# Optimization experiments

Hardware: AMD Instinct MI355X
Metric: run time of the kernel (lower is better)

Reference implementation:

```python
import jax, jax.numpy as jnp
import numpy as np

EMBED_DIM = 2048
NUM_HEADS = 16
B, L = 1, 4096


def setup_inputs() -> dict:
    key = jax.random.key(0)
    ks = jax.random.split(key, 6)
    s = 1.0 / np.sqrt(EMBED_DIM)
    return {
        "hidden_states": jax.random.normal(ks[0], (B, L, EMBED_DIM), jnp.float32),
        "Wq": jax.random.normal(ks[1], (EMBED_DIM, EMBED_DIM), jnp.float32) * s,
        "bq": jnp.zeros((EMBED_DIM,), jnp.float32),
        "Wk": jax.random.normal(ks[2], (EMBED_DIM, EMBED_DIM), jnp.float32) * s,
        "bk": jnp.zeros((EMBED_DIM,), jnp.float32),
        "Wv": jax.random.normal(ks[3], (EMBED_DIM, EMBED_DIM), jnp.float32) * s,
        "bv": jnp.zeros((EMBED_DIM,), jnp.float32),
        "Wo": jax.random.normal(ks[4], (EMBED_DIM, EMBED_DIM), jnp.float32) * s,
        "bo": jnp.zeros((EMBED_DIM,), jnp.float32),
        "is_causal": 1,
    }


def reference(hidden_states, Wq, bq, Wk, bk, Wv, bv, Wo, bo, is_causal):
    Bc, Lc, D = hidden_states.shape
    H = NUM_HEADS
    Dh = D // H
    scale = Dh ** (-0.5)

    def proj(W, b):
        # torch Linear: x @ W.T + b; reshape to [B, H, L, Dh]
        y = jnp.einsum('bld,ed->ble', hidden_states, W) + b
        return y.reshape(Bc, Lc, H, Dh).transpose(0, 2, 1, 3)

    q = proj(Wq, bq)
    k = proj(Wk, bk)
    v = proj(Wv, bv)

    scores = jnp.einsum('bhqd,bhkd->bhqk', q, k) * scale  # [B,H,L,L]
    if is_causal:
        causal = jnp.triu(jnp.ones((Lc, Lc), dtype=bool), k=1)
        scores = jnp.where(causal, -jnp.inf, scores)
    w = jax.nn.softmax(scores, axis=-1)
    attn = jnp.einsum('bhqk,bhkd->bhqd', w, v)
    attn = attn.transpose(0, 2, 1, 3).reshape(Bc, Lc, D)
    return jnp.einsum('bld,ed->ble', attn, Wo) + bo
```

## Files before the change

### kernel.cpp

```cpp
#include <hip/hip_runtime.h>
#include <hip/hip_bf16.h>

typedef unsigned short u16;
typedef __attribute__((ext_vector_type(8))) short short8;
typedef __attribute__((ext_vector_type(4))) float f32x4;

#define L 4096
#define DMODEL 2048
#define NHEADS 16
#define DHEAD 128
#define QSCALE (0.08838834764831845f * 1.44269504088896340f)

__device__ __forceinline__ u16 f2bf(float f){
  union { float f; unsigned int i; } v; v.f = f;
  unsigned int u = v.i;
  u += 0x7fffu + ((u >> 16) & 1u);
  return (u16)(u >> 16);
}

__device__ __forceinline__ unsigned int cvtpk(float lo, float hi){
  unsigned int d;
  asm("v_cvt_pk_bf16_f32 %0, %1, %2" : "=v"(d) : "v"(lo), "v"(hi));
  return d;
}

__global__ void cast_kernel(const float* __restrict__ in, u16* __restrict__ out, int n){
  int stride = gridDim.x * blockDim.x * 4;
  for (int j = (blockIdx.x * blockDim.x + threadIdx.x) * 4; j < n; j += stride){
    float4 f = *reinterpret_cast<const float4*>(in + j);
    ushort4 o;
    o.x = f2bf(f.x); o.y = f2bf(f.y); o.z = f2bf(f.z); o.w = f2bf(f.w);
    *reinterpret_cast<ushort4*>(out + j) = o;
  }
}

__global__ void cast_w4_kernel(const float* __restrict__ w0, const float* __restrict__ w1,
                               const float* __restrict__ w2, const float* __restrict__ w3,
                               u16* __restrict__ o0, u16* __restrict__ o1,
                               u16* __restrict__ o2, u16* __restrict__ o3){
  const float* in = (blockIdx.y == 0) ? w0 : (blockIdx.y == 1) ? w1 : (blockIdx.y == 2) ? w2 : w3;
  u16* out = (blockIdx.y == 0) ? o0 : (blockIdx.y == 1) ? o1 : (blockIdx.y == 2) ? o2 : o3;
  const int n = DMODEL * DMODEL;
  int stride = gridDim.x * blockDim.x * 4;
  for (int j = (blockIdx.x * blockDim.x + threadIdx.x) * 4; j < n; j += stride){
    float4 f = *reinterpret_cast<const float4*>(in + j);
    ushort4 o;
    o.x = f2bf(f.x); o.y = f2bf(f.y); o.z = f2bf(f.z); o.w = f2bf(f.w);
    *reinterpret_cast<ushort4*>(out + j) = o;
  }
}

__device__ __forceinline__ void gl_lds16(void* lds, const void* g){
  __builtin_amdgcn_global_load_lds(
      (const __attribute__((address_space(1))) unsigned int*)g,
      (__attribute__((address_space(3))) unsigned int*)lds, 16, 0, 0);
}

#define GBUF (24576)

__global__ __launch_bounds__(512, 2) void gemm_qkv(const u16* __restrict__ A,
    const u16* __restrict__ Wq, const u16* __restrict__ Wk, const u16* __restrict__ Wv,
    const float* __restrict__ bq, const float* __restrict__ bk, const float* __restrict__ bv,
    u16* __restrict__ Qb, u16* __restrict__ Kb, u16* __restrict__ Vtb){
  extern __shared__ u16 gsm[];
  const int tid = threadIdx.x;
  const int wid = tid >> 6, lane = tid & 63;
  const int wm = wid >> 2, wn = wid & 3;
  const int g = lane >> 4, r = lane & 15;
  const int bx = blockIdx.x;
  const int sel = blockIdx.y >> 4;
  const int byl = blockIdx.y & 15;

  const u16* W      = (sel == 0) ? Wq : (sel == 1) ? Wk : Wv;
  const float* bias = (sel == 0) ? bq : (sel == 1) ? bk : bv;
  const float cscale = (sel == 0) ? QSCALE : 1.0f;

  const int srow = tid >> 3;
  const int sc = ((tid & 7) * 16) ^ ((srow & 7) << 4);
  const u16* Ag = A + ((size_t)(bx * 256) + srow) * DMODEL + (sc >> 1);
  const u16* Bg = W + ((size_t)(byl * 128) + srow) * DMODEL + (sc >> 1);
  const int ldsw = wid * 1024;

  f32x4 acc[8][2];
  #pragma unroll
  for (int m = 0; m < 8; ++m){ acc[m][0] = (f32x4){0,0,0,0}; acc[m][1] = (f32x4){0,0,0,0}; }

  const int NK = DMODEL / 64;

  auto STAGE = [&](int b, int tk){
    char* ab = (char*)(gsm + b * GBUF);
    char* bb = (char*)(gsm + b * GBUF + 16384);
    const int ke = tk * 64;
    #pragma unroll
    for (int i = 0; i < 4; ++i)
      gl_lds16(ab + i * 8192 + ldsw, (const char*)(Ag + (size_t)i * 64 * DMODEL + ke));
    #pragma unroll
    for (int i = 0; i < 2; ++i)
      gl_lds16(bb + i * 8192 + ldsw, (const char*)(Bg + (size_t)i * 64 * DMODEL + ke));
  };

  STAGE(0, 0); STAGE(1, 1);

  for (int t = 0; t < NK; ++t){
    if (t < NK - 1) asm volatile("s_waitcnt vmcnt(6)" ::: "memory");
    else            asm volatile("s_waitcnt vmcnt(0)" ::: "memory");
    __builtin_amdgcn_sched_barrier(0);
    __builtin_amdgcn_s_barrier();
    __builtin_amdgcn_sched_barrier(0);

    if (t + 2 < NK) STAGE((t + 2) % 3, t + 2);

    const char* ab = (const char*)(gsm + (t % 3) * GBUF);
    const char* bb = (const char*)(gsm + (t % 3) * GBUF + 16384);

    short8 af[8][2], bf[2][2];
    #pragma unroll
    for (int mt = 0; mt < 8; ++mt){
      const int ar = wm * 128 + mt * 16 + r;
      #pragma unroll
      for (int ks = 0; ks < 2; ++ks)
        af[mt][ks] = *reinterpret_cast<const short8*>(
            ab + ar * 128 + ((ks * 64 + g * 16) ^ ((ar & 7) << 4)));
    }
    #pragma unroll
    for (int nt = 0; nt < 2; ++nt){
      const int br = wn * 32 + nt * 16 + r;
      #pragma unroll
      for (int ks = 0; ks < 2; ++ks)
        bf[nt][ks] = *reinterpret_cast<const short8*>(
            bb + br * 128 + ((ks * 64 + g * 16) ^ ((br & 7) << 4)));
    }

    __builtin_amdgcn_s_setprio(1);
    #pragma unroll
    for (int mt = 0; mt < 8; ++mt)
      #pragma unroll
      for (int nt = 0; nt < 2; ++nt)
        #pragma unroll
        for (int ks = 0; ks < 2; ++ks)
          acc[mt][nt] = __builtin_amdgcn_mfma_f32_16x16x32_bf16(af[mt][ks], bf[nt][ks], acc[mt][nt], 0, 0, 0);
    __builtin_amdgcn_s_setprio(0);
  }

  #pragma unroll
  for (int nt = 0; nt < 2; ++nt){
    const int col = byl * 128 + wn * 32 + nt * 16 + r;
    const float bv = bias[col];
    #pragma unroll
    for (int mt = 0; mt < 8; ++mt){
      #pragma unroll
      for (int qi = 0; qi < 4; ++qi){
        const int row = bx * 256 + wm * 128 + mt * 16 + g * 4 + qi;
        const u16 hb = f2bf((acc[mt][nt][qi] + bv) * cscale);
        if (sel < 2){
          u16* outp = (sel == 0) ? Qb : Kb;
          outp[(size_t)(col >> 7) * (L * DHEAD) + (size_t)row * DHEAD + (col & 127)] = hb;
        } else {
          Vtb[(size_t)(col >> 7) * (DHEAD * L) + (size_t)(col & 127) * L + row] = hb;
        }
      }
    }
  }
}

__global__ __launch_bounds__(512, 2) void gemm_o(const u16* __restrict__ A, const u16* __restrict__ W,
                                                 const float* __restrict__ bias, float* __restrict__ outp){
  extern __shared__ u16 gsm[];
  const int tid = threadIdx.x;
  const int wid = tid >> 6, lane = tid & 63;
  const int wm = wid >> 2, wn = wid & 3;
  const int g = lane >> 4, r = lane & 15;
  const int bx = blockIdx.x, by = blockIdx.y;

  const int srow = tid >> 3;
  const int sc = ((tid & 7) * 16) ^ ((srow & 7) << 4);
  const u16* Ag = A + ((size_t)(bx * 256) + srow) * DMODEL + (sc >> 1);
  const u16* Bg = W + ((size_t)(by * 128) + srow) * DMODEL + (sc >> 1);
  const int ldsw = wid * 1024;

  f32x4 acc[8][2];
  #pragma unroll
  for (int m = 0; m < 8; ++m){ acc[m][0] = (f32x4){0,0,0,0}; acc[m][1] = (f32x4){0,0,0,0}; }

  const int NK = DMODEL / 64;

  auto STAGE = [&](int b, int tk){
    char* ab = (char*)(gsm + b * GBUF);
    char* bb = (char*)(gsm + b * GBUF + 16384);
    const int ke = tk * 64;
    #pragma unroll
    for (int i = 0; i < 4; ++i)
      gl_lds16(ab + i * 8192 + ldsw, (const char*)(Ag + (size_t)i * 64 * DMODEL + ke));
    #pragma unroll
    for (int i = 0; i < 2; ++i)
      gl_lds16(bb + i * 8192 + ldsw, (const char*)(Bg + (size_t)i * 64 * DMODEL + ke));
  };

  STAGE(0, 0); STAGE(1, 1);

  for (int t = 0; t < NK; ++t){
    if (t < NK - 1) asm volatile("s_waitcnt vmcnt(6)" ::: "memory");
    else            asm volatile("s_waitcnt vmcnt(0)" ::: "memory");
    __builtin_amdgcn_sched_barrier(0);
    __builtin_amdgcn_s_barrier();
    __builtin_amdgcn_sched_barrier(0);

    if (t + 2 < NK) STAGE((t + 2) % 3, t + 2);

    const char* ab = (const char*)(gsm + (t % 3) * GBUF);
    const char* bb = (const char*)(gsm + (t % 3) * GBUF + 16384);

    short8 af[8][2], bf[2][2];
    #pragma unroll
    for (int mt = 0; mt < 8; ++mt){
      const int ar = wm * 128 + mt * 16 + r;
      #pragma unroll
      for (int ks = 0; ks < 2; ++ks)
        af[mt][ks] = *reinterpret_cast<const short8*>(
            ab + ar * 128 + ((ks * 64 + g * 16) ^ ((ar & 7) << 4)));
    }
    #pragma unroll
    for (int nt = 0; nt < 2; ++nt){
      const int br = wn * 32 + nt * 16 + r;
      #pragma unroll
      for (int ks = 0; ks < 2; ++ks)
        bf[nt][ks] = *reinterpret_cast<const short8*>(
            bb + br * 128 + ((ks * 64 + g * 16) ^ ((br & 7) << 4)));
    }

    __builtin_amdgcn_s_setprio(1);
    #pragma unroll
    for (int mt = 0; mt < 8; ++mt)
      #pragma unroll
      for (int nt = 0; nt < 2; ++nt)
        #pragma unroll
        for (int ks = 0; ks < 2; ++ks)
          acc[mt][nt] = __builtin_amdgcn_mfma_f32_16x16x32_bf16(af[mt][ks], bf[nt][ks], acc[mt][nt], 0, 0, 0);
    __builtin_amdgcn_s_setprio(0);
  }

  #pragma unroll
  for (int nt = 0; nt < 2; ++nt){
    const int col = by * 128 + wn * 32 + nt * 16 + r;
    const float bv = bias[col];
    #pragma unroll
    for (int mt = 0; mt < 8; ++mt){
      #pragma unroll
      for (int qi = 0; qi < 4; ++qi){
        const int row = bx * 256 + wm * 128 + mt * 16 + g * 4 + qi;
        outp[(size_t)row * DMODEL + col] = acc[mt][nt][qi] + bv;
      }
    }
  }
}


__device__ __forceinline__ void stage_K64(u16* buf, const u16* Kh, int kv0, int wid, int lane){
  #pragma unroll
  for (int i = 0; i < 4; ++i){
    int ib = (wid * 4 + i) * 1024;
    int off = ib + lane * 16;
    int row = off >> 8;
    int c = off & 255;
    int sc = c ^ ((row & 7) << 4);
    gl_lds16((char*)buf + ib, (const char*)(Kh + (size_t)(kv0 + row) * DHEAD) + sc);
  }
}

__device__ __forceinline__ void stage_V64(u16* buf, const u16* Vh, int kv0, int wid, int lane){
  #pragma unroll
  for (int i = 0; i < 4; ++i){
    int ib = (wid * 4 + i) * 1024;
    int off = ib + lane * 16;
    int row = off >> 7;
    int c = off & 127;
    int sc = c ^ ((row & 7) << 4);
    gl_lds16((char*)buf + ib, (const char*)(Vh + (size_t)row * L + kv0) + sc);
  }
}

__device__ __forceinline__ void sm_F(f32x4 (&s)[4], float &l, bool dg, int qrow,
                                     int kv0, int g, int r, char* Pw, int prow0){
  if (dg){
    #pragma unroll
    for (int cb = 0; cb < 4; ++cb){
      int kvb = kv0 + cb * 16 + g * 4;
      #pragma unroll
      for (int e = 0; e < 4; ++e)
        if (kvb + e > qrow) s[cb][e] = -1e30f;
    }
  }
  float rs = 0.f;
  uint2 pkv[4];
  #pragma unroll
  for (int cb = 0; cb < 4; ++cb){
    float p0 = __builtin_amdgcn_exp2f(s[cb][0]);
    float p1 = __builtin_amdgcn_exp2f(s[cb][1]);
    float p2 = __builtin_amdgcn_exp2f(s[cb][2]);
    float p3 = __builtin_amdgcn_exp2f(s[cb][3]);
    rs += (p0 + p1) + (p2 + p3);
    pkv[cb].x = cvtpk(p0, p1);
    pkv[cb].y = cvtpk(p2, p3);
  }
  rs += __shfl_xor(rs, 16);
  rs += __shfl_xor(rs, 32);
  l += rs;
  const int row = prow0 + r;
  char* base = Pw + row * 128;
  #pragma unroll
  for (int cb = 0; cb < 4; ++cb)
    *reinterpret_cast<uint2*>(base + ((cb * 32 + g * 8) ^ ((row & 7) << 4))) = pkv[cb];
}

__global__ __launch_bounds__(256, 2) void attn_kernel(const u16* __restrict__ Q, const u16* __restrict__ Km,
                                                      const u16* __restrict__ Vt, u16* __restrict__ Ob,
                                                      const int* __restrict__ is_causal_p){
  extern __shared__ u16 smem[];
  u16* Ks  = smem;
  u16* Vsm = smem + 16384;
  u16* Ps  = smem + 32768;

  const int lane = threadIdx.x & 63, wid = threadIdx.x >> 6;
  const int g = lane >> 4, r = lane & 15;

  int lg = (blockIdx.x & 7) * 64 + (blockIdx.x >> 3);
  int head = lg >> 5;
  int raw = lg & 31;
  int j = (head & 1) ? (31 - raw) : raw;
  const int jA = j, jB = 63 - j;
  const int causal = *is_causal_p;
  const int nt = causal ? (jB + 1) : 64;

  const u16* Qh = Q  + (size_t)head * L * DHEAD;
  const u16* Kh = Km + (size_t)head * L * DHEAD;
  const u16* Vh = Vt + (size_t)head * DHEAD * L;
  char* Pw = (char*)(Ps + wid * 2048);

  const int rowA = 64 * jA + wid * 16;
  const int rowB = 64 * jB + wid * 16;

  short8 qf[2][4];
  #pragma unroll
  for (int kb = 0; kb < 4; ++kb){
    qf[0][kb] = *reinterpret_cast<const short8*>(&Qh[(size_t)(rowA + r) * DHEAD + kb * 32 + g * 8]);
    qf[1][kb] = *reinterpret_cast<const short8*>(&Qh[(size_t)(rowB + r) * DHEAD + kb * 32 + g * 8]);
  }

  f32x4 o[2][8];
  #pragma unroll
  for (int m = 0; m < 2; ++m)
    #pragma unroll
    for (int db = 0; db < 8; ++db) o[m][db] = (f32x4){0.f, 0.f, 0.f, 0.f};
  float lA = 0.f, lB = 0.f;

  stage_K64(Ks,  Kh, 0, wid, lane);
  stage_V64(Vsm, Vh, 0, wid, lane);

  for (int t = 0; t < nt; ++t){
    const int kv0 = t * 64;
    const bool actA = (!causal) || (t <= jA);
    const bool dgA = causal && (t == jA);
    const bool dgB = causal && (t == jB);

    asm volatile("s_waitcnt vmcnt(0)" ::: "memory");
    __builtin_amdgcn_sched_barrier(0);
    __builtin_amdgcn_s_barrier();
    __builtin_amdgcn_sched_barrier(0);

    if (t + 1 < nt){
      stage_K64(Ks  + ((t + 1) & 1) * 8192, Kh, kv0 + 64, wid, lane);
      stage_V64(Vsm + ((t + 1) & 1) * 8192, Vh, kv0 + 64, wid, lane);
    }

    const char* Kb = (const char*)(Ks  + (t & 1) * 8192);
    const char* Vb = (const char*)(Vsm + (t & 1) * 8192);

    f32x4 s[2][4];
    #pragma unroll
    for (int m = 0; m < 2; ++m)
      #pragma unroll
      for (int cb = 0; cb < 4; ++cb) s[m][cb] = (f32x4){-16.f, -16.f, -16.f, -16.f};
    __builtin_amdgcn_s_setprio(1);
    #pragma unroll
    for (int cb = 0; cb < 4; ++cb){
      const int rr = cb * 16 + r;
      short8 kf[4];
      #pragma unroll
      for (int kb = 0; kb < 4; ++kb)
        kf[kb] = *reinterpret_cast<const short8*>(
            Kb + rr * 256 + ((kb * 64 + g * 16) ^ ((rr & 7) << 4)));
      if (actA){
        #pragma unroll
        for (int kb = 0; kb < 4; ++kb)
          s[0][cb] = __builtin_amdgcn_mfma_f32_16x16x32_bf16(kf[kb], qf[0][kb], s[0][cb], 0, 0, 0);
      }
      #pragma unroll
      for (int kb = 0; kb < 4; ++kb)
        s[1][cb] = __builtin_amdgcn_mfma_f32_16x16x32_bf16(kf[kb], qf[1][kb], s[1][cb], 0, 0, 0);
    }
    __builtin_amdgcn_s_setprio(0);

    if (actA) sm_F(s[0], lA, dgA, rowA + r, kv0, g, r, Pw, 0);
    sm_F(s[1], lB, dgB, rowB + r, kv0, g, r, Pw, 16);

    __builtin_amdgcn_s_setprio(1);
    #pragma unroll
    for (int st = 0; st < 2; ++st){
      short8 vf[8];
      #pragma unroll
      for (int db = 0; db < 8; ++db){
        const int rv = db * 16 + r;
        vf[db] = *reinterpret_cast<const short8*>(
            Vb + rv * 128 + (((st * 32 + g * 8) * 2) ^ ((rv & 7) << 4)));
      }
      if (st == 0){
        asm volatile("s_waitcnt lgkmcnt(0)" ::: "memory");
        __builtin_amdgcn_sched_barrier(0);
      }
      short8 pa0, pa1;
      if (actA)
        pa0 = *reinterpret_cast<const short8*>(
            Pw + r * 128 + ((st * 64 + g * 16) ^ ((r & 7) << 4)));
      pa1 = *reinterpret_cast<const short8*>(
          Pw + (16 + r) * 128 + ((st * 64 + g * 16) ^ ((r & 7) << 4)));
      #pragma unroll
      for (int db = 0; db < 8; ++db){
        if (actA)
          o[0][db] = __builtin_amdgcn_mfma_f32_16x16x32_bf16(pa0, vf[db], o[0][db], 0, 0, 0);
        o[1][db] = __builtin_amdgcn_mfma_f32_16x16x32_bf16(pa1, vf[db], o[1][db], 0, 0, 0);
      }
    }
    __builtin_amdgcn_s_setprio(0);
  }

  #pragma unroll
  for (int m = 0; m < 2; ++m){
    const int rbase = m ? rowB : rowA;
    const float lv = m ? lB : lA;
    float lb[4];
    #pragma unroll
    for (int qi = 0; qi < 4; ++qi) lb[qi] = __shfl(lv, g * 4 + qi);
    #pragma unroll
    for (int db = 0; db < 8; ++db)
      #pragma unroll
      for (int qi = 0; qi < 4; ++qi){
        float val = o[m][db][qi] / lb[qi];
        int qrow = rbase + g * 4 + qi;
        Ob[(size_t)qrow * DMODEL + head * DHEAD + db * 16 + r] = f2bf(val);
      }
  }
}

extern "C" void kernel_launch(void* const* d_in, const int* in_sizes, int n_in,
                              void* d_out, int out_size, void* d_ws, size_t ws_size,
                              hipStream_t stream){
  const float* X  = (const float*)d_in[0];
  const float* Wq = (const float*)d_in[1];
  const float* bq = (const float*)d_in[2];
  const float* Wk = (const float*)d_in[3];
  const float* bk = (const float*)d_in[4];
  const float* Wv = (const float*)d_in[5];
  const float* bv = (const float*)d_in[6];
  const float* Wo = (const float*)d_in[7];
  const float* bo = (const float*)d_in[8];
  const int*   isc = (const int*)d_in[9];

  char* ws = (char*)d_ws;
  u16* Xb  = (u16*)(ws);
  u16* Qb  = (u16*)(ws + 16777216);
  u16* Kb  = (u16*)(ws + 33554432);
  u16* Vtb = (u16*)(ws + 50331648);
  u16* Wqb = (u16*)(ws + 67108864);
  u16* Wkb = (u16*)(ws + 75497472);
  u16* Wvb = (u16*)(ws + 83886080);
  u16* Wob = (u16*)(ws + 92274688);
  u16* Ob  = Xb;

  (void)hipFuncSetAttribute(reinterpret_cast<const void*>(attn_kernel),
                            hipFuncAttributeMaxDynamicSharedMemorySize, 81920);
  (void)hipFuncSetAttribute(reinterpret_cast<const void*>(gemm_qkv),
                            hipFuncAttributeMaxDynamicSharedMemorySize, 147456);
  (void)hipFuncSetAttribute(reinterpret_cast<const void*>(gemm_o),
                            hipFuncAttributeMaxDynamicSharedMemorySize, 147456);

  cast_kernel<<<2048, 256, 0, stream>>>(X, Xb, L * DMODEL);
  cast_w4_kernel<<<dim3(1024, 4), 256, 0, stream>>>(Wq, Wk, Wv, Wo, Wqb, Wkb, Wvb, Wob);

  gemm_qkv<<<dim3(16, 48), 512, 147456, stream>>>(Xb, Wqb, Wkb, Wvb, bq, bk, bv, Qb, Kb, Vtb);

  attn_kernel<<<512, 256, 81920, stream>>>(Qb, Kb, Vtb, Ob, isc);

  gemm_o<<<dim3(16, 16), 512, 147456, stream>>>(Ob, Wob, bo, (float*)d_out);
}
```

Before: 299.7 us.

## Shrink attention KV tiles to 32 and split paired query blocks across waves

The attention kernel now uses 32-row KV tiles and 32-row query blocks. Instead of each wave handling both query blocks of a causal-balanced pair, two waves take the low block and two take the high block, each holding one Q fragment and one accumulator set. Shared memory drops to 36 KB, the grid doubles to 1024 blocks and launch bounds allow 4 blocks per CU, aiming for higher occupancy and lower register pressure. The cost is twice as many barrier iterations per unit of work, less K/V reuse per LDS load, and idle waves in the low-block half during steps past its causal limit.

```diff
diff --git a/kernel.cpp b/kernel.cpp
--- a/kernel.cpp
+++ b/kernel.cpp
@@ -255,10 +255,10 @@
 }
 
 
-__device__ __forceinline__ void stage_K64(u16* buf, const u16* Kh, int kv0, int wid, int lane){
-  #pragma unroll
-  for (int i = 0; i < 4; ++i){
-    int ib = (wid * 4 + i) * 1024;
+__device__ __forceinline__ void stage_K32(u16* buf, const u16* Kh, int kv0, int wid, int lane){
+  #pragma unroll
+  for (int i = 0; i < 2; ++i){
+    int ib = (wid * 2 + i) * 1024;
     int off = ib + lane * 16;
     int row = off >> 8;
     int c = off & 255;
@@ -267,23 +267,23 @@
   }
 }
 
-__device__ __forceinline__ void stage_V64(u16* buf, const u16* Vh, int kv0, int wid, int lane){
-  #pragma unroll
-  for (int i = 0; i < 4; ++i){
-    int ib = (wid * 4 + i) * 1024;
+__device__ __forceinline__ void stage_V32(u16* buf, const u16* Vh, int kv0, int wid, int lane){
+  #pragma unroll
+  for (int i = 0; i < 2; ++i){
+    int ib = (wid * 2 + i) * 1024;
     int off = ib + lane * 16;
-    int row = off >> 7;
-    int c = off & 127;
-    int sc = c ^ ((row & 7) << 4);
+    int row = off >> 6;
+    int c = off & 63;
+    int sc = c ^ ((row & 3) << 4);
     gl_lds16((char*)buf + ib, (const char*)(Vh + (size_t)row * L + kv0) + sc);
   }
 }
 
-__device__ __forceinline__ void sm_F(f32x4 (&s)[4], float &l, bool dg, int qrow,
-                                     int kv0, int g, int r, char* Pw, int prow0){
+__device__ __forceinline__ void sm_F(f32x4 (&s)[2], float &l, bool dg, int qrow,
+                                     int kv0, int g, int r, char* Pw){
   if (dg){
     #pragma unroll
-    for (int cb = 0; cb < 4; ++cb){
+    for (int cb = 0; cb < 2; ++cb){
       int kvb = kv0 + cb * 16 + g * 4;
       #pragma unroll
       for (int e = 0; e < 4; ++e)
@@ -291,9 +291,9 @@
     }
   }
   float rs = 0.f;
-  uint2 pkv[4];
-  #pragma unroll
-  for (int cb = 0; cb < 4; ++cb){
+  uint2 pkv[2];
+  #pragma unroll
+  for (int cb = 0; cb < 2; ++cb){
     float p0 = __builtin_amdgcn_exp2f(s[cb][0]);
     float p1 = __builtin_amdgcn_exp2f(s[cb][1]);
     float p2 = __builtin_amdgcn_exp2f(s[cb][2]);
@@ -305,62 +305,58 @@
   rs += __shfl_xor(rs, 16);
   rs += __shfl_xor(rs, 32);
   l += rs;
-  const int row = prow0 + r;
-  char* base = Pw + row * 128;
-  #pragma unroll
-  for (int cb = 0; cb < 4; ++cb)
-    *reinterpret_cast<uint2*>(base + ((cb * 32 + g * 8) ^ ((row & 7) << 4))) = pkv[cb];
-}
-
-__global__ __launch_bounds__(256, 2) void attn_kernel(const u16* __restrict__ Q, const u16* __restrict__ Km,
+  char* base = Pw + r * 64;
+  #pragma unroll
+  for (int cb = 0; cb < 2; ++cb)
+    *reinterpret_cast<uint2*>(base + ((cb * 32 + g * 8) ^ ((r & 3) << 4))) = pkv[cb];
+}
+
+__global__ __launch_bounds__(256, 4) void attn_kernel(const u16* __restrict__ Q, const u16* __restrict__ Km,
                                                       const u16* __restrict__ Vt, u16* __restrict__ Ob,
                                                       const int* __restrict__ is_causal_p){
   extern __shared__ u16 smem[];
   u16* Ks  = smem;
-  u16* Vsm = smem + 16384;
-  u16* Ps  = smem + 32768;
+  u16* Vsm = smem + 8192;
+  u16* Ps  = smem + 16384;
 
   const int lane = threadIdx.x & 63, wid = threadIdx.x >> 6;
   const int g = lane >> 4, r = lane & 15;
-
-  int lg = (blockIdx.x & 7) * 64 + (blockIdx.x >> 3);
-  int head = lg >> 5;
-  int raw = lg & 31;
-  int j = (head & 1) ? (31 - raw) : raw;
-  const int jA = j, jB = 63 - j;
+  const int sel = wid >> 1;
+  const int w2 = wid & 1;
+
+  int lg = (blockIdx.x & 7) * 128 + (blockIdx.x >> 3);
+  int head = lg >> 6;
+  int raw = lg & 63;
+  int j = (head & 1) ? (63 - raw) : raw;
+  const int jA = j, jB = 127 - j;
   const int causal = *is_causal_p;
-  const int nt = causal ? (jB + 1) : 64;
+  const int nt = causal ? (jB + 1) : (L / 32);
+  const int jlim = sel ? jB : jA;
 
   const u16* Qh = Q  + (size_t)head * L * DHEAD;
   const u16* Kh = Km + (size_t)head * L * DHEAD;
   const u16* Vh = Vt + (size_t)head * DHEAD * L;
-  char* Pw = (char*)(Ps + wid * 2048);
-
-  const int rowA = 64 * jA + wid * 16;
-  const int rowB = 64 * jB + wid * 16;
-
-  short8 qf[2][4];
-  #pragma unroll
-  for (int kb = 0; kb < 4; ++kb){
-    qf[0][kb] = *reinterpret_cast<const short8*>(&Qh[(size_t)(rowA + r) * DHEAD + kb * 32 + g * 8]);
-    qf[1][kb] = *reinterpret_cast<const short8*>(&Qh[(size_t)(rowB + r) * DHEAD + kb * 32 + g * 8]);
-  }
-
-  f32x4 o[2][8];
-  #pragma unroll
-  for (int m = 0; m < 2; ++m)
-    #pragma unroll
-    for (int db = 0; db < 8; ++db) o[m][db] = (f32x4){0.f, 0.f, 0.f, 0.f};
-  float lA = 0.f, lB = 0.f;
-
-  stage_K64(Ks,  Kh, 0, wid, lane);
-  stage_V64(Vsm, Vh, 0, wid, lane);
+  char* Pw = (char*)(Ps + wid * 512);
+
+  const int row0 = 32 * (sel ? jB : jA) + w2 * 16;
+
+  short8 qf[4];
+  #pragma unroll
+  for (int kb = 0; kb < 4; ++kb)
+    qf[kb] = *reinterpret_cast<const short8*>(&Qh[(size_t)(row0 + r) * DHEAD + kb * 32 + g * 8]);
+
+  f32x4 o[8];
+  #pragma unroll
+  for (int db = 0; db < 8; ++db) o[db] = (f32x4){0.f, 0.f, 0.f, 0.f};
+  float l = 0.f;
+
+  stage_K32(Ks,  Kh, 0, wid, lane);
+  stage_V32(Vsm, Vh, 0, wid, lane);
 
   for (int t = 0; t < nt; ++t){
-    const int kv0 = t * 64;
-    const bool actA = (!causal) || (t <= jA);
-    const bool dgA = causal && (t == jA);
-    const bool dgB = causal && (t == jB);
+    const int kv0 = t * 32;
+    const bool act = (!causal) || (t <= jlim);
+    const bool dg = causal && (t == jlim);
 
     asm volatile("s_waitcnt vmcnt(0)" ::: "memory");
     __builtin_amdgcn_sched_barrier(0);
@@ -368,87 +364,60 @@
     __builtin_amdgcn_sched_barrier(0);
 
     if (t + 1 < nt){
-      stage_K64(Ks  + ((t + 1) & 1) * 8192, Kh, kv0 + 64, wid, lane);
-      stage_V64(Vsm + ((t + 1) & 1) * 8192, Vh, kv0 + 64, wid, lane);
-    }
-
-    const char* Kb = (const char*)(Ks  + (t & 1) * 8192);
-    const char* Vb = (const char*)(Vsm + (t & 1) * 8192);
-
-    f32x4 s[2][4];
-    #pragma unroll
-    for (int m = 0; m < 2; ++m)
-      #pragma unroll
-      for (int cb = 0; cb < 4; ++cb) s[m][cb] = (f32x4){-16.f, -16.f, -16.f, -16.f};
-    __builtin_amdgcn_s_setprio(1);
-    #pragma unroll
-    for (int cb = 0; cb < 4; ++cb){
-      const int rr = cb * 16 + r;
-      short8 kf[4];
-      #pragma unroll
-      for (int kb = 0; kb < 4; ++kb)
-        kf[kb] = *reinterpret_cast<const short8*>(
-            Kb + rr * 256 + ((kb * 64 + g * 16) ^ ((rr & 7) << 4)));
-      if (actA){
+      stage_K32(Ks  + ((t + 1) & 1) * 4096, Kh, kv0 + 32, wid, lane);
+      stage_V32(Vsm + ((t + 1) & 1) * 4096, Vh, kv0 + 32, wid, lane);
+    }
+
+    if (act){
+      const char* Kb = (const char*)(Ks  + (t & 1) * 4096);
+      const char* Vb = (const char*)(Vsm + (t & 1) * 4096);
+
+      f32x4 s[2];
+      s[0] = (f32x4){-16.f, -16.f, -16.f, -16.f};
+      s[1] = (f32x4){-16.f, -16.f, -16.f, -16.f};
+      __builtin_amdgcn_s_setprio(1);
+      #pragma unroll
+      for (int cb = 0; cb < 2; ++cb){
+        const int rr = cb * 16 + r;
         #pragma unroll
-        for (int kb = 0; kb < 4; ++kb)
-          s[0][cb] = __builtin_amdgcn_mfma_f32_16x16x32_bf16(kf[kb], qf[0][kb], s[0][cb], 0, 0, 0);
+        for (int kb = 0; kb < 4; ++kb){
+          short8 kf = *reinterpret_cast<const short8*>(
+              Kb + rr * 256 + ((kb * 64 + g * 16) ^ ((rr & 7) << 4)));
+          s[cb] = __builtin_amdgcn_mfma_f32_16x16x32_bf16(kf, qf[kb], s[cb], 0, 0, 0);
+        }
       }
-      #pragma unroll
-      for (int kb = 0; kb < 4; ++kb)
-        s[1][cb] = __builtin_amdgcn_mfma_f32_16x16x32_bf16(kf[kb], qf[1][kb], s[1][cb], 0, 0, 0);
-    }
-    __builtin_amdgcn_s_setprio(0);
-
-    if (actA) sm_F(s[0], lA, dgA, rowA + r, kv0, g, r, Pw, 0);
-    sm_F(s[1], lB, dgB, rowB + r, kv0, g, r, Pw, 16);
-
-    __builtin_amdgcn_s_setprio(1);
-    #pragma unroll
-    for (int st = 0; st < 2; ++st){
-      short8 vf[8];
+      __builtin_amdgcn_s_setprio(0);
+
+      sm_F(s, l, dg, row0 + r, kv0, g, r, Pw);
+
+      asm volatile("s_waitcnt lgkmcnt(0)" ::: "memory");
+      __builtin_amdgcn_sched_barrier(0);
+
+      __builtin_amdgcn_s_setprio(1);
+      short8 pa = *reinterpret_cast<const short8*>(
+          Pw + r * 64 + ((g * 16) ^ ((r & 3) << 4)));
       #pragma unroll
       for (int db = 0; db < 8; ++db){
         const int rv = db * 16 + r;
-        vf[db] = *reinterpret_cast<const short8*>(
-            Vb + rv * 128 + (((st * 32 + g * 8) * 2) ^ ((rv & 7) << 4)));
+        short8 vf = *reinterpret_cast<const short8*>(
+            Vb + rv * 64 + ((g * 16) ^ ((rv & 3) << 4)));
+        o[db] = __builtin_amdgcn_mfma_f32_16x16x32_bf16(pa, vf, o[db], 0, 0, 0);
       }
-      if (st == 0){
-        asm volatile("s_waitcnt lgkmcnt(0)" ::: "memory");
-        __builtin_amdgcn_sched_barrier(0);
-      }
-      short8 pa0, pa1;
-      if (actA)
-        pa0 = *reinterpret_cast<const short8*>(
-            Pw + r * 128 + ((st * 64 + g * 16) ^ ((r & 7) << 4)));
-      pa1 = *reinterpret_cast<const short8*>(
-          Pw + (16 + r) * 128 + ((st * 64 + g * 16) ^ ((r & 7) << 4)));
-      #pragma unroll
-      for (int db = 0; db < 8; ++db){
-        if (actA)
-          o[0][db] = __builtin_amdgcn_mfma_f32_16x16x32_bf16(pa0, vf[db], o[0][db], 0, 0, 0);
-        o[1][db] = __builtin_amdgcn_mfma_f32_16x16x32_bf16(pa1, vf[db], o[1][db], 0, 0, 0);
-      }
-    }
-    __builtin_amdgcn_s_setprio(0);
-  }
-
-  #pragma unroll
-  for (int m = 0; m < 2; ++m){
-    const int rbase = m ? rowB : rowA;
-    const float lv = m ? lB : lA;
-    float lb[4];
-    #pragma unroll
-    for (int qi = 0; qi < 4; ++qi) lb[qi] = __shfl(lv, g * 4 + qi);
-    #pragma unroll
-    for (int db = 0; db < 8; ++db)
-      #pragma unroll
-      for (int qi = 0; qi < 4; ++qi){
-        float val = o[m][db][qi] / lb[qi];
-        int qrow = rbase + g * 4 + qi;
-        Ob[(size_t)qrow * DMODEL + head * DHEAD + db * 16 + r] = f2bf(val);
-      }
-  }
+      __builtin_amdgcn_s_setprio(0);
+    }
+  }
+
+  float lb[4];
+  #pragma unroll
+  for (int qi = 0; qi < 4; ++qi) lb[qi] = __shfl(l, g * 4 + qi);
+  #pragma unroll
+  for (int db = 0; db < 8; ++db)
+    #pragma unroll
+    for (int qi = 0; qi < 4; ++qi){
+      float val = o[db][qi] / lb[qi];
+      int qrow = row0 + g * 4 + qi;
+      Ob[(size_t)qrow * DMODEL + head * DHEAD + db * 16 + r] = f2bf(val);
+    }
 }
 
 extern "C" void kernel_launch(void* const* d_in, const int* in_sizes, int n_in,
@@ -477,7 +446,7 @@
   u16* Ob  = Xb;
 
   (void)hipFuncSetAttribute(reinterpret_cast<const void*>(attn_kernel),
-                            hipFuncAttributeMaxDynamicSharedMemorySize, 81920);
+                            hipFuncAttributeMaxDynamicSharedMemorySize, 36864);
   (void)hipFuncSetAttribute(reinterpret_cast<const void*>(gemm_qkv),
                             hipFuncAttributeMaxDynamicSharedMemorySize, 147456);
   (void)hipFuncSetAttribute(reinterpret_cast<const void*>(gemm_o),
@@ -488,7 +457,7 @@
 
   gemm_qkv<<<dim3(16, 48), 512, 147456, stream>>>(Xb, Wqb, Wkb, Wvb, bq, bk, bv, Qb, Kb, Vtb);
 
-  attn_kernel<<<512, 256, 81920, stream>>>(Qb, Kb, Vtb, Ob, isc);
+  attn_kernel<<<1024, 256, 36864, stream>>>(Qb, Kb, Vtb, Ob, isc);
 
   gemm_o<<<dim3(16, 16), 512, 147456, stream>>>(Ob, Wob, bo, (float*)d_out);
 }
```

Result: slower. 333.3 us (+11.2%).

## Keep softmax P in registers via permlane swaps and merge cast kernels

Applied to the files above, without the earlier changes.

Instead of writing the bf16 probability tile P to LDS and reading it back as the MFMA A-operand, the attention kernel rearranges P across lanes in registers with v_permlane32_swap and v_permlane16_swap. This removes the P round trip through LDS, the explicit lgkmcnt wait, and 16KB of shared memory per block. The V fragment loads are also interleaved with the MFMAs. Separately, the activation cast and the four weight casts are merged into one launch to save a kernel launch. The risk is extra cross-lane instructions, and that the register permutation must reproduce the MFMA operand layout exactly.

```diff
diff --git a/kernel.cpp b/kernel.cpp
--- a/kernel.cpp
+++ b/kernel.cpp
@@ -2,6 +2,7 @@
 #include <hip/hip_bf16.h>
 
 typedef unsigned short u16;
+typedef unsigned int u32;
 typedef __attribute__((ext_vector_type(8))) short short8;
 typedef __attribute__((ext_vector_type(4))) float f32x4;
 
@@ -18,29 +19,21 @@
   return (u16)(u >> 16);
 }
 
-__device__ __forceinline__ unsigned int cvtpk(float lo, float hi){
-  unsigned int d;
+__device__ __forceinline__ u32 cvtpk(float lo, float hi){
+  u32 d;
   asm("v_cvt_pk_bf16_f32 %0, %1, %2" : "=v"(d) : "v"(lo), "v"(hi));
   return d;
 }
 
-__global__ void cast_kernel(const float* __restrict__ in, u16* __restrict__ out, int n){
-  int stride = gridDim.x * blockDim.x * 4;
-  for (int j = (blockIdx.x * blockDim.x + threadIdx.x) * 4; j < n; j += stride){
-    float4 f = *reinterpret_cast<const float4*>(in + j);
-    ushort4 o;
-    o.x = f2bf(f.x); o.y = f2bf(f.y); o.z = f2bf(f.z); o.w = f2bf(f.w);
-    *reinterpret_cast<ushort4*>(out + j) = o;
-  }
-}
-
-__global__ void cast_w4_kernel(const float* __restrict__ w0, const float* __restrict__ w1,
-                               const float* __restrict__ w2, const float* __restrict__ w3,
-                               u16* __restrict__ o0, u16* __restrict__ o1,
-                               u16* __restrict__ o2, u16* __restrict__ o3){
-  const float* in = (blockIdx.y == 0) ? w0 : (blockIdx.y == 1) ? w1 : (blockIdx.y == 2) ? w2 : w3;
-  u16* out = (blockIdx.y == 0) ? o0 : (blockIdx.y == 1) ? o1 : (blockIdx.y == 2) ? o2 : o3;
-  const int n = DMODEL * DMODEL;
+__global__ void cast_all_kernel(const float* __restrict__ X, u16* __restrict__ Xo,
+                                const float* __restrict__ w0, const float* __restrict__ w1,
+                                const float* __restrict__ w2, const float* __restrict__ w3,
+                                u16* __restrict__ o0, u16* __restrict__ o1,
+                                u16* __restrict__ o2, u16* __restrict__ o3){
+  const int y = blockIdx.y;
+  const float* in = (y == 0) ? X : (y == 1) ? w0 : (y == 2) ? w1 : (y == 3) ? w2 : w3;
+  u16* out = (y == 0) ? Xo : (y == 1) ? o0 : (y == 2) ? o1 : (y == 3) ? o2 : o3;
+  const int n = (y == 0) ? (L * DMODEL) : (DMODEL * DMODEL);
   int stride = gridDim.x * blockDim.x * 4;
   for (int j = (blockIdx.x * blockDim.x + threadIdx.x) * 4; j < n; j += stride){
     float4 f = *reinterpret_cast<const float4*>(in + j);
@@ -279,8 +272,8 @@
   }
 }
 
-__device__ __forceinline__ void sm_F(f32x4 (&s)[4], float &l, bool dg, int qrow,
-                                     int kv0, int g, int r, char* Pw, int prow0){
+__device__ __forceinline__ void sm_R(f32x4 (&s)[4], float &l, bool dg, int qrow,
+                                     int kv0, int g, u32 (&paw)[2][4]){
   if (dg){
     #pragma unroll
     for (int cb = 0; cb < 4; ++cb){
@@ -291,7 +284,7 @@
     }
   }
   float rs = 0.f;
-  uint2 pkv[4];
+  u32 pk[4][2];
   #pragma unroll
   for (int cb = 0; cb < 4; ++cb){
     float p0 = __builtin_amdgcn_exp2f(s[cb][0]);
@@ -299,17 +292,23 @@
     float p2 = __builtin_amdgcn_exp2f(s[cb][2]);
     float p3 = __builtin_amdgcn_exp2f(s[cb][3]);
     rs += (p0 + p1) + (p2 + p3);
-    pkv[cb].x = cvtpk(p0, p1);
-    pkv[cb].y = cvtpk(p2, p3);
+    pk[cb][0] = cvtpk(p0, p1);
+    pk[cb][1] = cvtpk(p2, p3);
   }
   rs += __shfl_xor(rs, 16);
   rs += __shfl_xor(rs, 32);
   l += rs;
-  const int row = prow0 + r;
-  char* base = Pw + row * 128;
-  #pragma unroll
-  for (int cb = 0; cb < 4; ++cb)
-    *reinterpret_cast<uint2*>(base + ((cb * 32 + g * 8) ^ ((row & 7) << 4))) = pkv[cb];
+  #pragma unroll
+  for (int ks = 0; ks < 2; ++ks){
+    #pragma unroll
+    for (int h = 0; h < 2; ++h){
+      u32 a = pk[ks * 2][h], b = pk[ks * 2 + 1][h];
+      asm volatile("v_permlane32_swap_b32 %0, %1" : "+v"(a), "+v"(b));
+      asm volatile("v_permlane16_swap_b32 %0, %1" : "+v"(a), "+v"(b));
+      paw[ks][h] = a;
+      paw[ks][2 + h] = b;
+    }
+  }
 }
 
 __global__ __launch_bounds__(256, 2) void attn_kernel(const u16* __restrict__ Q, const u16* __restrict__ Km,
@@ -318,7 +317,6 @@
   extern __shared__ u16 smem[];
   u16* Ks  = smem;
   u16* Vsm = smem + 16384;
-  u16* Ps  = smem + 32768;
 
   const int lane = threadIdx.x & 63, wid = threadIdx.x >> 6;
   const int g = lane >> 4, r = lane & 15;
@@ -334,7 +332,6 @@
   const u16* Qh = Q  + (size_t)head * L * DHEAD;
   const u16* Kh = Km + (size_t)head * L * DHEAD;
   const u16* Vh = Vt + (size_t)head * DHEAD * L;
-  char* Pw = (char*)(Ps + wid * 2048);
 
   const int rowA = 64 * jA + wid * 16;
   const int rowB = 64 * jB + wid * 16;
@@ -400,34 +397,24 @@
     }
     __builtin_amdgcn_s_setprio(0);
 
-    if (actA) sm_F(s[0], lA, dgA, rowA + r, kv0, g, r, Pw, 0);
-    sm_F(s[1], lB, dgB, rowB + r, kv0, g, r, Pw, 16);
+    u32 pawA[2][4], pawB[2][4];
+    if (actA) sm_R(s[0], lA, dgA, rowA + r, kv0, g, pawA);
+    sm_R(s[1], lB, dgB, rowB + r, kv0, g, pawB);
 
     __builtin_amdgcn_s_setprio(1);
     #pragma unroll
     for (int st = 0; st < 2; ++st){
-      short8 vf[8];
+      union { u32 u[4]; short8 v; } pa0, pa1;
+      #pragma unroll
+      for (int w = 0; w < 4; ++w){ pa0.u[w] = pawA[st][w]; pa1.u[w] = pawB[st][w]; }
       #pragma unroll
       for (int db = 0; db < 8; ++db){
         const int rv = db * 16 + r;
-        vf[db] = *reinterpret_cast<const short8*>(
+        short8 vf = *reinterpret_cast<const short8*>(
             Vb + rv * 128 + (((st * 32 + g * 8) * 2) ^ ((rv & 7) << 4)));
-      }
-      if (st == 0){
-        asm volatile("s_waitcnt lgkmcnt(0)" ::: "memory");
-        __builtin_amdgcn_sched_barrier(0);
-      }
-      short8 pa0, pa1;
-      if (actA)
-        pa0 = *reinterpret_cast<const short8*>(
-            Pw + r * 128 + ((st * 64 + g * 16) ^ ((r & 7) << 4)));
-      pa1 = *reinterpret_cast<const short8*>(
-          Pw + (16 + r) * 128 + ((st * 64 + g * 16) ^ ((r & 7) << 4)));
-      #pragma unroll
-      for (int db = 0; db < 8; ++db){
         if (actA)
-          o[0][db] = __builtin_amdgcn_mfma_f32_16x16x32_bf16(pa0, vf[db], o[0][db], 0, 0, 0);
-        o[1][db] = __builtin_amdgcn_mfma_f32_16x16x32_bf16(pa1, vf[db], o[1][db], 0, 0, 0);
+          o[0][db] = __builtin_amdgcn_mfma_f32_16x16x32_bf16(pa0.v, vf, o[0][db], 0, 0, 0);
+        o[1][db] = __builtin_amdgcn_mfma_f32_16x16x32_bf16(pa1.v, vf, o[1][db], 0, 0, 0);
       }
     }
     __builtin_amdgcn_s_setprio(0);
@@ -477,18 +464,18 @@
   u16* Ob  = Xb;
 
   (void)hipFuncSetAttribute(reinterpret_cast<const void*>(attn_kernel),
-                            hipFuncAttributeMaxDynamicSharedMemorySize, 81920);
+                            hipFuncAttributeMaxDynamicSharedMemorySize, 65536);
   (void)hipFuncSetAttribute(reinterpret_cast<const void*>(gemm_qkv),
                             hipFuncAttributeMaxDynamicSharedMemorySize, 147456);
   (void)hipFuncSetAttribute(reinterpret_cast<const void*>(gemm_o),
                             hipFuncAttributeMaxDynamicSharedMemorySize, 147456);
 
-  cast_kernel<<<2048, 256, 0, stream>>>(X, Xb, L * DMODEL);
-  cast_w4_kernel<<<dim3(1024, 4), 256, 0, stream>>>(Wq, Wk, Wv, Wo, Wqb, Wkb, Wvb, Wob);
+  cast_all_kernel<<<dim3(1024, 5), 256, 0, stream>>>(X, Xb, Wq, Wk, Wv, Wo,
+                                                     Wqb, Wkb, Wvb, Wob);
 
   gemm_qkv<<<dim3(16, 48), 512, 147456, stream>>>(Xb, Wqb, Wkb, Wvb, bq, bk, bv, Qb, Kb, Vtb);
 
-  attn_kernel<<<512, 256, 81920, stream>>>(Qb, Kb, Vtb, Ob, isc);
+  attn_kernel<<<512, 256, 65536, stream>>>(Qb, Kb, Vtb, Ob, isc);
 
   gemm_o<<<dim3(16, 16), 512, 147456, stream>>>(Ob, Wob, bo, (float*)d_out);
 }
```

Measured after the change: 293.1 us. -2.2%, faster.
